# Kernel optimization log

Hardware: AMD Instinct MI355X
Metric: run time of the kernel (lower is better)

The kernel has to match this reference:

```python
import jax, jax.numpy as jnp
import numpy as np


def conv1x1(x, w, b):
    # x: [B,C,H,W], w: [O,C], b: [O]
    return jnp.einsum('bchw,oc->bohw', x, w) + b[None, :, None, None]


def dwconv(x, w):
    # depthwise conv, x: [B,C,H,W], w: [C,1,k,k], SAME padding (k odd, pad=k//2)
    return jax.lax.conv_general_dilated(
        x, w, window_strides=(1, 1), padding='SAME',
        dimension_numbers=('NCHW', 'OIHW', 'NCHW'),
        feature_group_count=x.shape[1])


def setup_inputs() -> dict:
    key = jax.random.key(0)
    ks = jax.random.split(key, 14)
    B, C, H, W = 16, 256, 64, 64
    OC = C // 16  # scale=16 -> 16
    WSCALE = 0.05
    r = lambda k, shape: jax.random.normal(k, shape, dtype=jnp.float32) * WSCALE
    return {
        'x': jax.random.normal(ks[0], (B, C, H, W), dtype=jnp.float32),
        'conv_w': r(ks[1], (C + 4, C)),           # 1x1 conv -> ctx (C) + gates (3+1)
        'conv_b': r(ks[2], (C + 4,)),
        'fw3': r(ks[3], (C, 1, 3, 3)),            # depthwise focal kernels
        'fw5': r(ks[4], (C, 1, 5, 5)),
        'fw7': r(ks[5], (C, 1, 7, 7)),
        'key_w': r(ks[6], (1, C)),                # Conv_key 1x1
        'key_b': r(ks[7], (1,)),
        'v1_w': r(ks[8], (OC, C)),                # Conv_value first 1x1
        'v1_b': r(ks[9], (OC,)),
        'ln_w': jnp.ones((OC,), dtype=jnp.float32),
        'ln_b': jnp.zeros((OC,), dtype=jnp.float32),
        'v2_w': r(ks[10], (C, OC)),               # Conv_value second 1x1
        'v2_b': r(ks[11], (C,)),
    }


def reference(x, conv_w, conv_b, fw3, fw5, fw7, key_w, key_b,
              v1_w, v1_b, ln_w, ln_b, v2_w, v2_b):
    B, C, H, W = x.shape
    # _contextAggregation
    t = conv1x1(x, conv_w, conv_b)          # [B, C+4, H, W]
    ctx, gates = t[:, :C], t[:, C:]         # [B,C,H,W], [B,4,H,W]
    ctx_all = jnp.zeros_like(ctx)
    for l, fw in enumerate((fw3, fw5, fw7)):
        ctx = jax.nn.gelu(dwconv(ctx, fw), approximate=False)  # torch GELU = exact erf
        ctx_all = ctx_all + ctx * gates[:, l:l + 1]
    ctx_global = jnp.mean(ctx, axis=(2, 3), keepdims=True)     # AdaptiveAvgPool2d(1)
    ctx_all = ctx_all + ctx_global * gates[:, 3:4]
    # GC-style channel attention: softmax over spatial positions
    k = conv1x1(ctx_all, key_w, key_b).reshape(B, H * W)       # [B, HW]
    k = jax.nn.softmax(k, axis=1)
    q = ctx_all.reshape(B, C, H * W)
    qk = jnp.einsum('bcn,bn->bc', q, k)[:, :, None, None]      # [B,C,1,1]
    # Conv_value: 1x1 -> LayerNorm([OC,1,1]) -> ReLU -> 1x1
    v = conv1x1(qk, v1_w, v1_b)                                # [B,OC,1,1]
    mu = jnp.mean(v, axis=(1, 2, 3), keepdims=True)
    var = jnp.var(v, axis=(1, 2, 3), keepdims=True)
    v = (v - mu) * jax.lax.rsqrt(var + 1e-5)
    v = v * ln_w[None, :, None, None] + ln_b[None, :, None, None]
    v = jax.nn.relu(v)
    v = conv1x1(v, v2_w, v2_b)                                 # [B,C,1,1]
    return ctx_all + v
```

## Files before the change

kernel.cpp:

```cpp
#include <hip/hip_runtime.h>

#define DEVFN __device__ __forceinline__

constexpr int B  = 16;
constexpr int C  = 256;
constexpr int N  = 64 * 64;
constexpr int O1 = C + 4;

typedef __attribute__((ext_vector_type(8)))  short bf16x8;
typedef __attribute__((ext_vector_type(4)))  short bf16x4;
typedef __attribute__((ext_vector_type(16))) float f32x16;
typedef unsigned short ushort_t;

DEVFN short f2bf(float f){
  union { float f; unsigned u; } p; p.f = f;
  unsigned r = p.u + 0x7fffu + ((p.u >> 16) & 1u);
  return (short)(r >> 16);
}
DEVFN unsigned pack2(float lo, float hi){
  return (unsigned)(ushort_t)f2bf(lo) | ((unsigned)(ushort_t)f2bf(hi) << 16);
}
DEVFN float lo2f(unsigned u){ union{unsigned u; float f;} p; p.u = u << 16; return p.f; }
DEVFN float hi2f(unsigned u){ union{unsigned u; float f;} p; p.u = u & 0xffff0000u; return p.f; }
DEVFN float bf2f(ushort_t s){ union{unsigned u; float f;} p; p.u = (unsigned)s << 16; return p.f; }

DEVFN float gelu_fast(float x){
  float y = 1.5957691216f * fmaf(0.044715f * x * x, x, x);
  float s = __builtin_amdgcn_rcpf(1.0f + __expf(-y));
  return x * s;
}

__global__ __launch_bounds__(256, 4)
void k_conv1_mfma(const float* __restrict__ x, const float* __restrict__ w,
                  const float* __restrict__ bias, ushort_t* __restrict__ ctxb,
                  float* __restrict__ gates){
  __shared__ __align__(16) short wlds[16 * 64 * 8];
  __shared__ __align__(16) short xlds[16 * 64 * 8];
  const int tid  = threadIdx.x;
  const int wv   = tid >> 6;
  const int lane = tid & 63;
  const int l31  = lane & 31;
  const int lhi  = lane >> 5;
  const int oBase = blockIdx.y * 64;
  const int pg0   = blockIdx.x * 64;
  const int b  = pg0 >> 12;
  const int n0 = pg0 & 4095;
  const int mw = (wv >> 1) * 32;
  const int nw = (wv & 1) * 32;

  const int rstage = tid & 63;
  const int kg0    = (tid >> 6) * 4;
  const int oS     = oBase + rstage;
  const float* wpb = w + oS * 256;
  const float* xpb = x + (size_t)b * C * N + n0 + rstage;

  f32x16 acc;
  #pragma unroll
  for(int r = 0; r < 16; r++) acc[r] = 0.f;

  unsigned wpkA[16], xpkA[16], wpkB[16], xpkB[16];

  auto loadW = [&](int kc, unsigned* wpk){
    #pragma unroll
    for(int t = 0; t < 4; t++){
      const int kg = kg0 + t;
      if(oS < O1){
        const float4 f0 = *(const float4*)(wpb + kc + kg * 8);
        const float4 f1 = *(const float4*)(wpb + kc + kg * 8 + 4);
        wpk[t*4+0] = pack2(f0.x, f0.y); wpk[t*4+1] = pack2(f0.z, f0.w);
        wpk[t*4+2] = pack2(f1.x, f1.y); wpk[t*4+3] = pack2(f1.z, f1.w);
      } else {
        wpk[t*4+0] = wpk[t*4+1] = wpk[t*4+2] = wpk[t*4+3] = 0u;
      }
    }
  };
  auto loadX = [&](int kc, unsigned* xpk){
    #pragma unroll
    for(int t = 0; t < 4; t++){
      const int kg = kg0 + t;
      const float* xp = xpb + (size_t)(kc + kg * 8) * N;
      float f[8];
      #pragma unroll
      for(int j = 0; j < 8; j++) f[j] = xp[(size_t)j * N];
      xpk[t*4+0] = pack2(f[0], f[1]); xpk[t*4+1] = pack2(f[2], f[3]);
      xpk[t*4+2] = pack2(f[4], f[5]); xpk[t*4+3] = pack2(f[6], f[7]);
    }
  };
  auto storeLDS = [&](const unsigned* wpk, const unsigned* xpk){
    #pragma unroll
    for(int t = 0; t < 4; t++){
      const int kg = kg0 + t;
      uint4 wq; wq.x = wpk[t*4+0]; wq.y = wpk[t*4+1]; wq.z = wpk[t*4+2]; wq.w = wpk[t*4+3];
      uint4 xq; xq.x = xpk[t*4+0]; xq.y = xpk[t*4+1]; xq.z = xpk[t*4+2]; xq.w = xpk[t*4+3];
      *(uint4*)&wlds[(kg * 64 + rstage) * 8] = wq;
      *(uint4*)&xlds[(kg * 64 + rstage) * 8] = xq;
    }
  };
  auto mfma8 = [&](){
    #pragma unroll
    for(int ks = 0; ks < 8; ks++){
      const int kg = ks * 2 + lhi;
      bf16x8 af  = *(const bf16x8*)&wlds[(kg * 64 + mw + l31) * 8];
      bf16x8 bfr = *(const bf16x8*)&xlds[(kg * 64 + nw + l31) * 8];
      acc = __builtin_amdgcn_mfma_f32_32x32x16_bf16(af, bfr, acc, 0, 0, 0);
    }
  };

  loadW(0, wpkA); loadX(0, xpkA);
  storeLDS(wpkA, xpkA);
  __syncthreads();
  loadW(128, wpkB); loadX(128, xpkB);
  mfma8();
  __syncthreads();
  storeLDS(wpkB, xpkB);
  __syncthreads();
  mfma8();

  const int n = n0 + nw + l31;
  #pragma unroll
  for(int r = 0; r < 16; r++){
    const int row = (r & 3) + 8 * (r >> 2) + 4 * lhi;
    const int o = oBase + mw + row;
    if(o >= O1) continue;
    const float v = acc[r] + bias[o];
    if(o < 256)
      ctxb[((size_t)(b * 256 + o)) * N + n] = (ushort_t)f2bf(v);
    else
      gates[((size_t)(b * 4 + (o - 256))) * N + n] = v;
  }
}

constexpr int SSTR = 72;

DEVFN void unpack16(const short* p, float* wnd){
  uint4 a = *(const uint4*)p;
  uint4 b = *(const uint4*)(p + 8);
  unsigned ua[8] = {a.x, a.y, a.z, a.w, b.x, b.y, b.z, b.w};
  #pragma unroll
  for(int d = 0; d < 8; d++){ wnd[2*d] = lo2f(ua[d]); wnd[2*d+1] = hi2f(ua[d]); }
}

template<int K>
DEVFN void dw_stage(const short* src, const float* __restrict__ fw, int c,
                    int h, int w0, float* val){
  constexpr int R = K / 2;
  float acc[8];
  #pragma unroll
  for(int i = 0; i < 8; i++) acc[i] = 0.f;
  #pragma unroll
  for(int ky = 0; ky < K; ky++){
    const int r = h + ky - R;
    if((unsigned)r < 64u){
      float wnd[16];
      unpack16(&src[r * SSTR + w0], wnd);
      #pragma unroll
      for(int kx = 0; kx < K; kx++){
        const float wv = fw[c * K * K + ky * K + kx];
        #pragma unroll
        for(int i = 0; i < 8; i++)
          acc[i] = fmaf(wnd[i + kx + 4 - R], wv, acc[i]);
      }
    }
  }
  #pragma unroll
  for(int i = 0; i < 8; i++) val[i] = gelu_fast(acc[i]);
}

DEVFN void store_row(short* dst, int h, int w0, const float* val){
  bf16x4 lo, hi;
  #pragma unroll
  for(int i = 0; i < 4; i++){ lo[i] = f2bf(val[i]); hi[i] = f2bf(val[i + 4]); }
  *(bf16x4*)&dst[h * SSTR + w0 + 4] = lo;
  *(bf16x4*)&dst[h * SSTR + w0 + 8] = hi;
}

__global__ __launch_bounds__(512, 8)
void k_dwchain(ushort_t* __restrict__ ctxb, const float* __restrict__ fw3,
               const float* __restrict__ fw5, const float* __restrict__ fw7,
               const float* __restrict__ gates){
  __shared__ __align__(16) short bufA[64 * SSTR];
  __shared__ __align__(16) short bufB[64 * SSTR];
  __shared__ float wred[8];
  const int tid = threadIdx.x;
  const int plane = blockIdx.x;
  const int b = plane >> 8;
  const int c = plane & 255;
  const int h  = tid >> 3;
  const int w0 = (tid & 7) * 8;
  const int nbase = h * 64 + w0;

  if(tid < 64){
    bf16x4 z = {0, 0, 0, 0};
    *(bf16x4*)&bufA[tid * SSTR] = z;  *(bf16x4*)&bufA[tid * SSTR + 68] = z;
    *(bf16x4*)&bufB[tid * SSTR] = z;  *(bf16x4*)&bufB[tid * SSTR + 68] = z;
  }
  {
    bf16x8 iv = *(const bf16x8*)((const short*)ctxb + (size_t)plane * N + tid * 8);
    bf16x4 lo, hi;
    #pragma unroll
    for(int j = 0; j < 4; j++){ lo[j] = iv[j]; hi[j] = iv[j + 4]; }
    *(bf16x4*)&bufA[h * SSTR + w0 + 4] = lo;
    *(bf16x4*)&bufA[h * SSTR + w0 + 8] = hi;
  }
  __syncthreads();

  float ctxp[8];
  #pragma unroll
  for(int i = 0; i < 8; i++) ctxp[i] = 0.f;
  float val[8];

  dw_stage<3>(bufA, fw3, c, h, w0, val);
  {
    const float* gp = gates + ((size_t)(b * 4 + 0)) * N + nbase;
    float4 ga = *(const float4*)gp, gb = *(const float4*)(gp + 4);
    ctxp[0] = fmaf(val[0], ga.x, ctxp[0]); ctxp[1] = fmaf(val[1], ga.y, ctxp[1]);
    ctxp[2] = fmaf(val[2], ga.z, ctxp[2]); ctxp[3] = fmaf(val[3], ga.w, ctxp[3]);
    ctxp[4] = fmaf(val[4], gb.x, ctxp[4]); ctxp[5] = fmaf(val[5], gb.y, ctxp[5]);
    ctxp[6] = fmaf(val[6], gb.z, ctxp[6]); ctxp[7] = fmaf(val[7], gb.w, ctxp[7]);
    store_row(bufB, h, w0, val);
  }
  __syncthreads();

  dw_stage<5>(bufB, fw5, c, h, w0, val);
  {
    const float* gp = gates + ((size_t)(b * 4 + 1)) * N + nbase;
    float4 ga = *(const float4*)gp, gb = *(const float4*)(gp + 4);
    ctxp[0] = fmaf(val[0], ga.x, ctxp[0]); ctxp[1] = fmaf(val[1], ga.y, ctxp[1]);
    ctxp[2] = fmaf(val[2], ga.z, ctxp[2]); ctxp[3] = fmaf(val[3], ga.w, ctxp[3]);
    ctxp[4] = fmaf(val[4], gb.x, ctxp[4]); ctxp[5] = fmaf(val[5], gb.y, ctxp[5]);
    ctxp[6] = fmaf(val[6], gb.z, ctxp[6]); ctxp[7] = fmaf(val[7], gb.w, ctxp[7]);
    store_row(bufA, h, w0, val);
  }
  __syncthreads();

  dw_stage<7>(bufA, fw7, c, h, w0, val);
  float lsum = 0.f;
  {
    const float* gp = gates + ((size_t)(b * 4 + 2)) * N + nbase;
    float4 ga = *(const float4*)gp, gb = *(const float4*)(gp + 4);
    ctxp[0] = fmaf(val[0], ga.x, ctxp[0]); ctxp[1] = fmaf(val[1], ga.y, ctxp[1]);
    ctxp[2] = fmaf(val[2], ga.z, ctxp[2]); ctxp[3] = fmaf(val[3], ga.w, ctxp[3]);
    ctxp[4] = fmaf(val[4], gb.x, ctxp[4]); ctxp[5] = fmaf(val[5], gb.y, ctxp[5]);
    ctxp[6] = fmaf(val[6], gb.z, ctxp[6]); ctxp[7] = fmaf(val[7], gb.w, ctxp[7]);
    #pragma unroll
    for(int i = 0; i < 8; i++) lsum += val[i];
  }
  #pragma unroll
  for(int off = 32; off > 0; off >>= 1) lsum += __shfl_xor(lsum, off, 64);
  if((tid & 63) == 0) wred[tid >> 6] = lsum;
  __syncthreads();
  float mean = 0.f;
  #pragma unroll
  for(int i = 0; i < 8; i++) mean += wred[i];
  mean *= (1.0f / 4096.0f);

  {
    const float* gp = gates + ((size_t)(b * 4 + 3)) * N + nbase;
    float4 ga = *(const float4*)gp, gb = *(const float4*)(gp + 4);
    bf16x8 ov;
    ov[0] = f2bf(fmaf(mean, ga.x, ctxp[0])); ov[1] = f2bf(fmaf(mean, ga.y, ctxp[1]));
    ov[2] = f2bf(fmaf(mean, ga.z, ctxp[2])); ov[3] = f2bf(fmaf(mean, ga.w, ctxp[3]));
    ov[4] = f2bf(fmaf(mean, gb.x, ctxp[4])); ov[5] = f2bf(fmaf(mean, gb.y, ctxp[5]));
    ov[6] = f2bf(fmaf(mean, gb.z, ctxp[6])); ov[7] = f2bf(fmaf(mean, gb.w, ctxp[7]));
    *(bf16x8*)((short*)ctxb + (size_t)plane * N + nbase) = ov;
  }
}

__global__ __launch_bounds__(256)
void k_logits(const ushort_t* __restrict__ P, const float* __restrict__ key_w,
              const float* __restrict__ key_b, float* __restrict__ logits){
  __shared__ float kw[256];
  __shared__ float part[512];
  int tid = threadIdx.x;
  kw[tid] = key_w[tid];
  __syncthreads();
  int b  = blockIdx.x >> 5;
  int n0 = (blockIdx.x & 31) * 128;
  int cpart = tid >> 6, pxp = tid & 63;
  const ushort_t* pp = P + ((size_t)(b * 256 + cpart * 64)) * N + n0 + pxp * 2;
  float a0 = 0.f, a1 = 0.f;
  #pragma unroll 8
  for(int c = 0; c < 64; c++){
    unsigned u = *(const unsigned*)(pp + (size_t)c * N);
    float kwv = kw[cpart * 64 + c];
    a0 = fmaf(lo2f(u), kwv, a0);
    a1 = fmaf(hi2f(u), kwv, a1);
  }
  part[cpart * 128 + pxp * 2]     = a0;
  part[cpart * 128 + pxp * 2 + 1] = a1;
  __syncthreads();
  if(tid < 128){
    float l = part[tid] + part[128 + tid] + part[256 + tid] + part[384 + tid];
    logits[b * N + n0 + tid] = l + key_b[0];
  }
}

__global__ __launch_bounds__(1024)
void k_softmax(float* __restrict__ kbuf){
  __shared__ float wred[16];
  int b = blockIdx.x, tid = threadIdx.x;
  const int wave = tid >> 6, lane = tid & 63;
  float v[4];
  float m = -1e30f;
  #pragma unroll
  for(int i = 0; i < 4; i++){
    v[i] = kbuf[b * N + tid + i * 1024];
    m = fmaxf(m, v[i]);
  }
  #pragma unroll
  for(int off = 32; off > 0; off >>= 1) m = fmaxf(m, __shfl_xor(m, off, 64));
  if(lane == 0) wred[wave] = m;
  __syncthreads();
  float mm = -1e30f;
  #pragma unroll
  for(int i = 0; i < 16; i++) mm = fmaxf(mm, wred[i]);
  __syncthreads();
  float s = 0.f;
  #pragma unroll
  for(int i = 0; i < 4; i++){ v[i] = __expf(v[i] - mm); s += v[i]; }
  #pragma unroll
  for(int off = 32; off > 0; off >>= 1) s += __shfl_xor(s, off, 64);
  if(lane == 0) wred[wave] = s;
  __syncthreads();
  float tot = 0.f;
  #pragma unroll
  for(int i = 0; i < 16; i++) tot += wred[i];
  float inv = 1.0f / tot;
  #pragma unroll
  for(int i = 0; i < 4; i++)
    kbuf[b * N + tid + i * 1024] = v[i] * inv;
}

__global__ __launch_bounds__(256)
void k_qk(const ushort_t* __restrict__ P, const float* __restrict__ kbuf,
          float* __restrict__ qk){
  __shared__ float red[256];
  int plane = blockIdx.x, tid = threadIdx.x;
  int b = plane >> 8;
  const unsigned* pp = (const unsigned*)(P + (size_t)plane * N);
  const float2* kp = (const float2*)(kbuf + b * N);
  float acc = 0.f;
  #pragma unroll
  for(int i = 0; i < 8; i++){
    int idx = tid + i * 256;
    unsigned u = pp[idx];
    float2 kk = kp[idx];
    acc = fmaf(lo2f(u), kk.x, acc);
    acc = fmaf(hi2f(u), kk.y, acc);
  }
  red[tid] = acc; __syncthreads();
  for(int s = 128; s > 0; s >>= 1){
    if(tid < s) red[tid] += red[tid + s];
    __syncthreads();
  }
  if(tid == 0) qk[plane] = red[0];
}

__global__ __launch_bounds__(256)
void k_v(const float* __restrict__ qk, const float* __restrict__ v1w,
         const float* __restrict__ v1b, const float* __restrict__ lnw,
         const float* __restrict__ lnb, const float* __restrict__ v2w,
         const float* __restrict__ v2b, float* __restrict__ vout){
  int b = blockIdx.x, tid = threadIdx.x;
  __shared__ float qs[256];
  __shared__ float part[256];
  __shared__ float v1s[16];
  __shared__ float vr[16];
  __shared__ float stats[2];
  qs[tid] = qk[b * 256 + tid];
  __syncthreads();
  int oc = tid >> 4, ln = tid & 15;
  float p = 0.f;
  #pragma unroll
  for(int j = 0; j < 16; j++){
    int cc = ln + j * 16;
    p = fmaf(v1w[oc * 256 + cc], qs[cc], p);
  }
  part[tid] = p;
  __syncthreads();
  if(tid < 16){
    float s = v1b[tid];
    for(int j = 0; j < 16; j++) s += part[tid * 16 + j];
    v1s[tid] = s;
  }
  __syncthreads();
  if(tid == 0){
    float mu = 0.f;
    for(int i = 0; i < 16; i++) mu += v1s[i];
    mu *= (1.f / 16.f);
    float var = 0.f;
    for(int i = 0; i < 16; i++){ float d = v1s[i] - mu; var += d * d; }
    var *= (1.f / 16.f);
    stats[0] = mu; stats[1] = rsqrtf(var + 1e-5f);
  }
  __syncthreads();
  if(tid < 16){
    float vv = (v1s[tid] - stats[0]) * stats[1] * lnw[tid] + lnb[tid];
    vr[tid] = fmaxf(vv, 0.f);
  }
  __syncthreads();
  float o = v2b[tid];
  #pragma unroll
  for(int j = 0; j < 16; j++) o = fmaf(v2w[tid * 16 + j], vr[j], o);
  vout[b * 256 + tid] = o;
}

__global__ __launch_bounds__(256)
void k_final(float* __restrict__ out, const ushort_t* __restrict__ ctxb,
             const float* __restrict__ vout){
  int idx8 = blockIdx.x * 256 + threadIdx.x;
  int plane = idx8 >> 9;
  int off = (idx8 & 511) * 8;
  bf16x8 v = *(const bf16x8*)((const short*)ctxb + (size_t)plane * N + off);
  float vv = vout[plane];
  float4 o0, o1;
  o0.x = bf2f((ushort_t)v[0]) + vv; o0.y = bf2f((ushort_t)v[1]) + vv;
  o0.z = bf2f((ushort_t)v[2]) + vv; o0.w = bf2f((ushort_t)v[3]) + vv;
  o1.x = bf2f((ushort_t)v[4]) + vv; o1.y = bf2f((ushort_t)v[5]) + vv;
  o1.z = bf2f((ushort_t)v[6]) + vv; o1.w = bf2f((ushort_t)v[7]) + vv;
  float* op = out + (size_t)plane * N + off;
  *(float4*)op = o0;
  *(float4*)(op + 4) = o1;
}

extern "C" void kernel_launch(void* const* d_in, const int* in_sizes, int n_in,
                              void* d_out, int out_size, void* d_ws, size_t ws_size,
                              hipStream_t stream){
  const float* x      = (const float*)d_in[0];
  const float* conv_w = (const float*)d_in[1];
  const float* conv_b = (const float*)d_in[2];
  const float* fw3    = (const float*)d_in[3];
  const float* fw5    = (const float*)d_in[4];
  const float* fw7    = (const float*)d_in[5];
  const float* key_w  = (const float*)d_in[6];
  const float* key_b  = (const float*)d_in[7];
  const float* v1_w   = (const float*)d_in[8];
  const float* v1_b   = (const float*)d_in[9];
  const float* ln_w   = (const float*)d_in[10];
  const float* ln_b   = (const float*)d_in[11];
  const float* v2_w   = (const float*)d_in[12];
  const float* v2_b   = (const float*)d_in[13];
  float* out = (float*)d_out;

  const size_t PL = (size_t)B * C * N;
  char* p = (char*)d_ws;
  ushort_t* ctxb = (ushort_t*)p;  p += PL * sizeof(ushort_t);
  float* gates   = (float*)p;     p += (size_t)B * 4 * N * sizeof(float);
  float* kbuf    = (float*)p;     p += (size_t)B * N * sizeof(float);
  float* qkb     = (float*)p;     p += (size_t)B * C * sizeof(float);
  float* vout    = (float*)p;

  k_conv1_mfma<<<dim3(1024, 5), 256, 0, stream>>>(x, conv_w, conv_b, ctxb, gates);
  k_dwchain<<<B * C, 512, 0, stream>>>(ctxb, fw3, fw5, fw7, gates);
  k_logits<<<512, 256, 0, stream>>>(ctxb, key_w, key_b, kbuf);
  k_softmax<<<B, 1024, 0, stream>>>(kbuf);
  k_qk<<<B * C, 256, 0, stream>>>(ctxb, kbuf, qkb);
  k_v<<<B, 256, 0, stream>>>(qkb, v1_w, v1_b, ln_w, ln_b, v2_w, v2_b, vout);
  k_final<<<8192, 256, 0, stream>>>(out, ctxb, vout);
}
```

Measured before the change: 296.6 us.

## Compute all output channels per block and pre-convert 1x1 weights to bf16

The first 1x1 conv kernel now has each block cover all 320 (padded) output channels for a 64-pixel tile, instead of splitting output channels across 5 grid rows. Each x tile is then read from global memory and converted to bf16 once, not five times. A small pre-kernel converts conv_w to bf16 once per call, so blocks load packed weights directly. The K loop becomes four 64-wide stages with register prefetch of x, and occupancy drops to 3 blocks per SIMD cluster because each wave now holds 5 accumulator tiles and LDS use is larger.

```diff
diff --git a/kernel.cpp b/kernel.cpp
--- a/kernel.cpp
+++ b/kernel.cpp
@@ -30,103 +30,123 @@
   return x * s;
 }
 
-__global__ __launch_bounds__(256, 4)
-void k_conv1_mfma(const float* __restrict__ x, const float* __restrict__ w,
+__global__ __launch_bounds__(256)
+void k_wbf(const float* __restrict__ w, ushort_t* __restrict__ wbf){
+  int idx = blockIdx.x * 256 + threadIdx.x;
+  int o = idx >> 8, cc = idx & 255;
+  wbf[idx] = (o < O1) ? (ushort_t)f2bf(w[o * 256 + cc]) : (ushort_t)0;
+}
+
+__global__ __launch_bounds__(256, 3)
+void k_conv1_mfma(const float* __restrict__ x, const ushort_t* __restrict__ wbf,
                   const float* __restrict__ bias, ushort_t* __restrict__ ctxb,
                   float* __restrict__ gates){
-  __shared__ __align__(16) short wlds[16 * 64 * 8];
-  __shared__ __align__(16) short xlds[16 * 64 * 8];
+  __shared__ __align__(16) short wlds[8 * 320 * 8];
+  __shared__ __align__(16) short xlds[8 * 64 * 8];
+  __shared__ float sbias[320];
   const int tid  = threadIdx.x;
-  const int wv   = tid >> 6;
+  const int wave = tid >> 6;
   const int lane = tid & 63;
   const int l31  = lane & 31;
   const int lhi  = lane >> 5;
-  const int oBase = blockIdx.y * 64;
-  const int pg0   = blockIdx.x * 64;
-  const int b  = pg0 >> 12;
-  const int n0 = pg0 & 4095;
-  const int mw = (wv >> 1) * 32;
-  const int nw = (wv & 1) * 32;
-
-  const int rstage = tid & 63;
-  const int kg0    = (tid >> 6) * 4;
-  const int oS     = oBase + rstage;
-  const float* wpb = w + oS * 256;
-  const float* xpb = x + (size_t)b * C * N + n0 + rstage;
-
-  f32x16 acc;
-  #pragma unroll
-  for(int r = 0; r < 16; r++) acc[r] = 0.f;
-
-  unsigned wpkA[16], xpkA[16], wpkB[16], xpkB[16];
-
-  auto loadW = [&](int kc, unsigned* wpk){
-    #pragma unroll
-    for(int t = 0; t < 4; t++){
-      const int kg = kg0 + t;
-      if(oS < O1){
-        const float4 f0 = *(const float4*)(wpb + kc + kg * 8);
-        const float4 f1 = *(const float4*)(wpb + kc + kg * 8 + 4);
-        wpk[t*4+0] = pack2(f0.x, f0.y); wpk[t*4+1] = pack2(f0.z, f0.w);
-        wpk[t*4+2] = pack2(f1.x, f1.y); wpk[t*4+3] = pack2(f1.z, f1.w);
-      } else {
-        wpk[t*4+0] = wpk[t*4+1] = wpk[t*4+2] = wpk[t*4+3] = 0u;
+  const int pg0  = blockIdx.x * 64;
+  const int b    = pg0 >> 12;
+  const int n0   = pg0 & 4095;
+  const int nwv  = (wave & 1) * 32;
+  const int mrow = wave >> 1;
+
+  sbias[tid] = bias[tid];
+  if(tid < 64) sbias[256 + tid] = (256 + tid < O1) ? bias[256 + tid] : 0.f;
+
+  const float* xpb = x + (size_t)b * C * N + n0;
+
+  f32x16 acc[5];
+  #pragma unroll
+  for(int t = 0; t < 5; t++)
+    #pragma unroll
+    for(int r = 0; r < 16; r++) acc[t][r] = 0.f;
+
+  float xf[2][8];
+
+  auto pfX = [&](int kc){
+    #pragma unroll
+    for(int p = 0; p < 2; p++){
+      const int idx = p * 256 + tid;
+      const int kg = idx >> 6, n = idx & 63;
+      const float* xp = xpb + (size_t)(kc + kg * 8) * N + n;
+      #pragma unroll
+      for(int j = 0; j < 8; j++) xf[p][j] = xp[(size_t)j * N];
+    }
+  };
+  auto stX = [&](){
+    #pragma unroll
+    for(int p = 0; p < 2; p++){
+      const int idx = p * 256 + tid;
+      const int kg = idx >> 6, n = idx & 63;
+      uint4 v;
+      v.x = pack2(xf[p][0], xf[p][1]); v.y = pack2(xf[p][2], xf[p][3]);
+      v.z = pack2(xf[p][4], xf[p][5]); v.w = pack2(xf[p][6], xf[p][7]);
+      *(uint4*)&xlds[(kg * 64 + n) * 8] = v;
+    }
+  };
+  auto stW = [&](int kc){
+    #pragma unroll
+    for(int q = 0; q < 10; q++){
+      const int pidx = q * 256 + tid;
+      const int kg = pidx / 320;
+      const int m  = pidx - kg * 320;
+      uint4 v = *(const uint4*)(wbf + (size_t)m * 256 + kc + kg * 8);
+      *(uint4*)&wlds[(kg * 320 + m) * 8] = v;
+    }
+  };
+  auto mfmaC = [&](){
+    #pragma unroll
+    for(int ks = 0; ks < 4; ks++){
+      const int kg = ks * 2 + lhi;
+      bf16x8 bfr = *(const bf16x8*)&xlds[(kg * 64 + nwv + l31) * 8];
+      #pragma unroll
+      for(int t = 0; t < 5; t++){
+        const int m0 = (mrow + 2 * t) * 32;
+        bf16x8 af = *(const bf16x8*)&wlds[(kg * 320 + m0 + l31) * 8];
+        acc[t] = __builtin_amdgcn_mfma_f32_32x32x16_bf16(af, bfr, acc[t], 0, 0, 0);
       }
     }
   };
-  auto loadX = [&](int kc, unsigned* xpk){
-    #pragma unroll
-    for(int t = 0; t < 4; t++){
-      const int kg = kg0 + t;
-      const float* xp = xpb + (size_t)(kc + kg * 8) * N;
-      float f[8];
-      #pragma unroll
-      for(int j = 0; j < 8; j++) f[j] = xp[(size_t)j * N];
-      xpk[t*4+0] = pack2(f[0], f[1]); xpk[t*4+1] = pack2(f[2], f[3]);
-      xpk[t*4+2] = pack2(f[4], f[5]); xpk[t*4+3] = pack2(f[6], f[7]);
-    }
-  };
-  auto storeLDS = [&](const unsigned* wpk, const unsigned* xpk){
-    #pragma unroll
-    for(int t = 0; t < 4; t++){
-      const int kg = kg0 + t;
-      uint4 wq; wq.x = wpk[t*4+0]; wq.y = wpk[t*4+1]; wq.z = wpk[t*4+2]; wq.w = wpk[t*4+3];
-      uint4 xq; xq.x = xpk[t*4+0]; xq.y = xpk[t*4+1]; xq.z = xpk[t*4+2]; xq.w = xpk[t*4+3];
-      *(uint4*)&wlds[(kg * 64 + rstage) * 8] = wq;
-      *(uint4*)&xlds[(kg * 64 + rstage) * 8] = xq;
-    }
-  };
-  auto mfma8 = [&](){
-    #pragma unroll
-    for(int ks = 0; ks < 8; ks++){
-      const int kg = ks * 2 + lhi;
-      bf16x8 af  = *(const bf16x8*)&wlds[(kg * 64 + mw + l31) * 8];
-      bf16x8 bfr = *(const bf16x8*)&xlds[(kg * 64 + nw + l31) * 8];
-      acc = __builtin_amdgcn_mfma_f32_32x32x16_bf16(af, bfr, acc, 0, 0, 0);
-    }
-  };
-
-  loadW(0, wpkA); loadX(0, xpkA);
-  storeLDS(wpkA, xpkA);
-  __syncthreads();
-  loadW(128, wpkB); loadX(128, xpkB);
-  mfma8();
-  __syncthreads();
-  storeLDS(wpkB, xpkB);
-  __syncthreads();
-  mfma8();
-
-  const int n = n0 + nw + l31;
-  #pragma unroll
-  for(int r = 0; r < 16; r++){
-    const int row = (r & 3) + 8 * (r >> 2) + 4 * lhi;
-    const int o = oBase + mw + row;
-    if(o >= O1) continue;
-    const float v = acc[r] + bias[o];
-    if(o < 256)
-      ctxb[((size_t)(b * 256 + o)) * N + n] = (ushort_t)f2bf(v);
-    else
-      gates[((size_t)(b * 4 + (o - 256))) * N + n] = v;
+
+  stW(0); pfX(0); stX();
+  __syncthreads();
+  pfX(64);
+  mfmaC();
+  __syncthreads();
+  stW(64); stX();
+  __syncthreads();
+  pfX(128);
+  mfmaC();
+  __syncthreads();
+  stW(128); stX();
+  __syncthreads();
+  pfX(192);
+  mfmaC();
+  __syncthreads();
+  stW(192); stX();
+  __syncthreads();
+  mfmaC();
+
+  const int n = n0 + nwv + l31;
+  #pragma unroll
+  for(int t = 0; t < 5; t++){
+    const int mt = (mrow + 2 * t) * 32;
+    #pragma unroll
+    for(int r = 0; r < 16; r++){
+      const int row = (r & 3) + 8 * (r >> 2) + 4 * lhi;
+      const int o = mt + row;
+      if(o >= O1) continue;
+      const float v = acc[t][r] + sbias[o];
+      if(o < 256)
+        ctxb[((size_t)(b * 256 + o)) * N + n] = (ushort_t)f2bf(v);
+      else
+        gates[((size_t)(b * 4 + (o - 256))) * N + n] = v;
+    }
   }
 }
 
@@ -448,9 +468,11 @@
   float* gates   = (float*)p;     p += (size_t)B * 4 * N * sizeof(float);
   float* kbuf    = (float*)p;     p += (size_t)B * N * sizeof(float);
   float* qkb     = (float*)p;     p += (size_t)B * C * sizeof(float);
-  float* vout    = (float*)p;
-
-  k_conv1_mfma<<<dim3(1024, 5), 256, 0, stream>>>(x, conv_w, conv_b, ctxb, gates);
+  float* vout    = (float*)p;     p += (size_t)B * C * sizeof(float);
+  ushort_t* wbf  = (ushort_t*)p;
+
+  k_wbf<<<320, 256, 0, stream>>>(conv_w, wbf);
+  k_conv1_mfma<<<1024, 256, 0, stream>>>(x, wbf, conv_b, ctxb, gates);
   k_dwchain<<<B * C, 512, 0, stream>>>(ctxb, fw3, fw5, fw7, gates);
   k_logits<<<512, 256, 0, stream>>>(ctxb, key_w, key_b, kbuf);
   k_softmax<<<B, 1024, 0, stream>>>(kbuf);
```

Result: faster. 283.6 us (-4.4%).
